# Kernel tuning notes

Measured on AMD Instinct MI355X. Metric: run time of the kernel, lower is better.

## Reference

```python
import jax, jax.numpy as jnp
import numpy as np

N_NODES = 50000
N_EDGES = 1600000
IN_FEATS = 128
HIDDEN = 32
HEADS = 4
N_GRAPHS = 64
NEG_SLOPE = 0.2


def setup_inputs() -> dict:
    key = jax.random.key(0)
    ks = jax.random.split(key, 10)
    features = jax.random.normal(ks[0], (N_NODES, IN_FEATS), dtype=jnp.float32)
    src = jax.random.randint(ks[1], (N_EDGES,), 0, N_NODES, dtype=jnp.int32)
    dst = jax.random.randint(ks[2], (N_EDGES,), 0, N_NODES, dtype=jnp.int32)
    graph_ids = jnp.sort(jax.random.randint(ks[3], (N_NODES,), 0, N_GRAPHS, dtype=jnp.int32))
    # GATConv params (fc has no bias in DGL; conv bias added post-aggregation)
    s = 1.0 / np.sqrt(IN_FEATS)
    W = jax.random.uniform(ks[4], (IN_FEATS, HEADS * HIDDEN), jnp.float32, -s, s)
    attn_l = jax.random.normal(ks[5], (HEADS, HIDDEN), dtype=jnp.float32) * 0.1
    attn_r = jax.random.normal(ks[6], (HEADS, HIDDEN), dtype=jnp.float32) * 0.1
    bias = jnp.zeros((HEADS * HIDDEN,), dtype=jnp.float32)
    s2 = 1.0 / np.sqrt(HEADS * HIDDEN)
    fc_w = jax.random.uniform(ks[7], (HEADS * HIDDEN, 1), jnp.float32, -s2, s2)
    fc_b = jnp.zeros((1,), dtype=jnp.float32)
    return dict(features=features, src=src, dst=dst, graph_ids=graph_ids,
                W=W, attn_l=attn_l, attn_r=attn_r, bias=bias, fc_w=fc_w, fc_b=fc_b)


def reference(features, src, dst, graph_ids, W, attn_l, attn_r, bias, fc_w, fc_b):
    N = features.shape[0]
    H, D = attn_l.shape
    feat = (features @ W).reshape(N, H, D)              # [N,H,D]
    el = jnp.sum(feat * attn_l[None], axis=-1)          # [N,H]
    er = jnp.sum(feat * attn_r[None], axis=-1)          # [N,H]
    e = jax.nn.leaky_relu(el[src] + er[dst], NEG_SLOPE) # [E,H]
    # edge softmax over incoming edges of each dst node
    m = jax.ops.segment_max(e, dst, num_segments=N)     # [N,H]
    ex = jnp.exp(e - m[dst])
    denom = jax.ops.segment_sum(ex, dst, num_segments=N)
    a = ex / denom[dst]                                 # [E,H]
    msg = feat[src] * a[:, :, None]                     # [E,H,D]
    rst = jax.ops.segment_sum(msg, dst, num_segments=N) # [N,H,D]
    h = rst.reshape(N, H * D) + bias[None, :]
    # dropout(p=0.5) treated as identity (eval mode)
    h = jax.nn.elu(h)
    counts = jax.ops.segment_sum(jnp.ones((N,), h.dtype), graph_ids, num_segments=N_GRAPHS)
    hg = jax.ops.segment_sum(h, graph_ids, num_segments=N_GRAPHS) / counts[:, None]
    y = jax.nn.sigmoid(hg @ fc_w + fc_b[None, :])       # [G,1]
    return y
```

## Files before the change

kernel.cpp:

```cpp
#include <hip/hip_runtime.h>
#include <hip/hip_bf16.h>
#include <math.h>

#define N_NODES 50000
#define N_EDGES 1600000
#define HEADS 4
#define HIDDEN 32
#define N_GRAPHS 64
#define NEG_SLOPE 0.2f

#define NBUCK 196
#define BKT_EPT 8
#define BKT_CHUNK (256 * BKT_EPT)
#define NBKB ((N_EDGES + BKT_CHUNK - 1) / BKT_CHUNK)

#define OFS_FEAT 0
#define OFS_EBUF 0
#define OFS_EL   6400000
#define OFS_ER   6600000
#define OFS_P    6800000
#define OFS_GCNT 6850000
#define OFS_GBASE 6850256
#define OFS_GPOS 6850512
#define OFS_WAB  6850768
#define OFS_OFF  6900000
#define OFS_SRC  6950272

typedef __attribute__((ext_vector_type(8))) short short8;
typedef __attribute__((ext_vector_type(4))) float f32x4;

#define LDS_S 68

__device__ __forceinline__ unsigned pack_bf16x2(float a, float b) {
  __hip_bfloat16 ha = __float2bfloat16(a), hb = __float2bfloat16(b);
  unsigned ua = *(const unsigned short*)&ha, ub = *(const unsigned short*)&hb;
  return ua | (ub << 16);
}
__device__ __forceinline__ float bf16_lo(unsigned u) {
  unsigned v = u << 16; return *(const float*)&v;
}
__device__ __forceinline__ float bf16_hi(unsigned u) {
  unsigned v = u & 0xFFFF0000u; return *(const float*)&v;
}

__global__ __launch_bounds__(1024) void k_wab(const float* __restrict__ W,
                                              const float* __restrict__ al,
                                              const float* __restrict__ ar,
                                              float* __restrict__ wab) {
  int t = threadIdx.x;
  int k = t >> 3, c = t & 7;
  int h = c & 3;
  const float* av = (c < 4) ? al : ar;
  float s = 0.f;
  for (int d = 0; d < 32; ++d)
    s = fmaf(W[k * 128 + h * 32 + d], av[h * 32 + d], s);
  wab[k * 8 + c] = s;
}

__global__ __launch_bounds__(256, 2) void k_gemm(
    const float* __restrict__ X, const float* __restrict__ W,
    const float* __restrict__ wab, unsigned* __restrict__ featb,
    float* __restrict__ el, float* __restrict__ er) {
  __shared__ unsigned Wt[144 * LDS_S];
  __shared__ unsigned Xt[64 * LDS_S];
  const int t = threadIdx.x;
  const int lane = t & 63;
  const int wv = t >> 6;
  const int nb0 = blockIdx.x * 64;

  {
    const int c = t & 127;
    const int ph = (t >> 7) * 32;
    for (int p = ph; p < ph + 32; ++p)
      Wt[c * LDS_S + p] = pack_bf16x2(W[(2 * p) * 128 + c], W[(2 * p + 1) * 128 + c]);
  }
  if (t < 128) {
    const int c = t & 7;
    const int p0 = (t >> 3) * 4;
    for (int q = 0; q < 4; ++q) {
      int p = p0 + q;
      Wt[(128 + c) * LDS_S + p] =
          pack_bf16x2(wab[(2 * p) * 8 + c], wab[(2 * p + 1) * 8 + c]);
    }
  } else {
    const int c = (t - 128) & 7;
    const int p0 = ((t - 128) >> 3) * 4;
    for (int q = 0; q < 4; ++q) Wt[(136 + c) * LDS_S + p0 + q] = 0;
  }
  {
    const int row = t >> 2;
    const int c0 = (t & 3) * 32;
    const int node = nb0 + row;
    const float4* xs = (const float4*)(X + (size_t)node * 128 + c0);
    for (int i = 0; i < 8; ++i) {
      float4 v = make_float4(0.f, 0.f, 0.f, 0.f);
      if (node < N_NODES) v = xs[i];
      int p = (c0 >> 1) + i * 2;
      Xt[row * LDS_S + p] = pack_bf16x2(v.x, v.y);
      Xt[row * LDS_S + p + 1] = pack_bf16x2(v.z, v.w);
    }
  }
  __syncthreads();

  const int rrow = lane & 15;
  const int rgrp = lane >> 4;
  f32x4 acc[9];
#pragma unroll
  for (int i = 0; i < 9; ++i) acc[i] = (f32x4){0.f, 0.f, 0.f, 0.f};
  const int arow = wv * 16 + rrow;

#pragma unroll
  for (int kk = 0; kk < 4; ++kk) {
    const int pbase = kk * 16 + rgrp * 4;
    short8 afrag = *(const short8*)&Xt[arow * LDS_S + pbase];
#pragma unroll
    for (int bt = 0; bt < 9; ++bt) {
      short8 bfrag = *(const short8*)&Wt[(bt * 16 + rrow) * LDS_S + pbase];
      acc[bt] = __builtin_amdgcn_mfma_f32_16x16x32_bf16(afrag, bfrag, acc[bt], 0, 0, 0);
    }
  }

  const int nodebase = nb0 + wv * 16 + rgrp * 4;
#pragma unroll
  for (int bt = 0; bt < 8; ++bt) {
#pragma unroll
    for (int j = 0; j < 4; ++j) {
      float other = __shfl_xor(acc[bt][j], 1, 64);
      if ((lane & 1) == 0) {
        int node = nodebase + j;
        if (node < N_NODES)
          featb[(size_t)node * 64 + bt * 8 + (rrow >> 1)] =
              pack_bf16x2(acc[bt][j], other);
      }
    }
  }
#pragma unroll
  for (int j = 0; j < 4; ++j) {
    int node = nodebase + j;
    if (node < N_NODES) {
      if (rrow < 4) el[node * 4 + rrow] = acc[8][j];
      else if (rrow < 8) er[node * 4 + (rrow - 4)] = acc[8][j];
    }
  }
}

__global__ void k_bhist(const int* __restrict__ dst, int* __restrict__ gcount) {
  __shared__ int lh[NBUCK];
  const int t = threadIdx.x;
  if (t < NBUCK) lh[t] = 0;
  __syncthreads();
  const int base = blockIdx.x * BKT_CHUNK;
#pragma unroll
  for (int j = 0; j < BKT_EPT; ++j) {
    int e = base + j * 256 + t;
    if (e < N_EDGES) atomicAdd(&lh[dst[e] >> 8], 1);
  }
  __syncthreads();
  if (t < NBUCK && lh[t] > 0) atomicAdd(&gcount[t], lh[t]);
}

__global__ void k_bscan(const int* __restrict__ gcount, int* __restrict__ gbase,
                        int* __restrict__ gpos) {
  __shared__ int sh[256];
  const int t = threadIdx.x;
  int v = (t < NBUCK) ? gcount[t] : 0;
  sh[t] = v;
  __syncthreads();
  for (int s = 1; s < 256; s <<= 1) {
    int add = (t >= s) ? sh[t - s] : 0;
    __syncthreads();
    sh[t] += add;
    __syncthreads();
  }
  int excl = sh[t] - v;
  if (t < NBUCK) { gbase[t] = excl; gpos[t] = excl; }
  if (t == NBUCK - 1) gbase[NBUCK] = excl + v;
}

__global__ void k_bucket(const int* __restrict__ src, const int* __restrict__ dst,
                         int* __restrict__ gpos, int2* __restrict__ ebuf) {
  __shared__ int lh[NBUCK];
  __shared__ int lbase[NBUCK];
  const int t = threadIdx.x;
  if (t < NBUCK) lh[t] = 0;
  __syncthreads();
  const int base = blockIdx.x * BKT_CHUNK;
  int s8[BKT_EPT], d8[BKT_EPT], r8[BKT_EPT], b8[BKT_EPT];
#pragma unroll
  for (int j = 0; j < BKT_EPT; ++j) {
    int e = base + j * 256 + t;
    bool ok = e < N_EDGES;
    s8[j] = ok ? src[e] : 0;
    d8[j] = ok ? dst[e] : 0;
    b8[j] = d8[j] >> 8;
    int r = 0;
    if (ok) r = atomicAdd(&lh[b8[j]], 1);
    r8[j] = r;
  }
  __syncthreads();
  if (t < NBUCK && lh[t] > 0) lbase[t] = atomicAdd(&gpos[t], lh[t]);
  __syncthreads();
#pragma unroll
  for (int j = 0; j < BKT_EPT; ++j) {
    int e = base + j * 256 + t;
    if (e < N_EDGES) ebuf[lbase[b8[j]] + r8[j]] = make_int2(s8[j], d8[j]);
  }
}

__global__ __launch_bounds__(1024) void k_bsort(
    const int2* __restrict__ ebuf, const int* __restrict__ gbase,
    int* __restrict__ srcbuf, int* __restrict__ off) {
  __shared__ int lcnt[256];
  __shared__ int loff[256];
  __shared__ int lpos[256];
  const int t = threadIdx.x;
  const int b = blockIdx.x;
  const int lo = gbase[b], hi = gbase[b + 1];
  if (t < 256) lcnt[t] = 0;
  __syncthreads();
  for (int i = lo + t; i < hi; i += 1024)
    atomicAdd(&lcnt[ebuf[i].y & 255], 1);
  __syncthreads();
  int v = (t < 256) ? lcnt[t] : 0;
  if (t < 256) loff[t] = v;
  __syncthreads();
  for (int s = 1; s < 256; s <<= 1) {
    int add = (t >= s && t < 256) ? loff[t - s] : 0;
    __syncthreads();
    if (t < 256) loff[t] += add;
    __syncthreads();
  }
  if (t < 256) {
    int excl = loff[t] - v;
    lpos[t] = excl;
    int node = b * 256 + t;
    if (node < N_NODES) off[node] = lo + excl;
  }
  if (b == NBUCK - 1 && t == 0) off[N_NODES] = N_EDGES;
  __syncthreads();
  for (int i = lo + t; i < hi; i += 1024) {
    int2 e = ebuf[i];
    int p = atomicAdd(&lpos[e.y & 255], 1);
    srcbuf[lo + p] = e.x;
  }
}

__global__ __launch_bounds__(256) void k_aggregate(
    const unsigned* __restrict__ featb, const float* __restrict__ el,
    const float* __restrict__ er, const int* __restrict__ off,
    const int* __restrict__ srcbuf, const float* __restrict__ bias,
    const float* __restrict__ fc_w, float* __restrict__ pbuf) {
  int gid = blockIdx.x * blockDim.x + threadIdx.x;
  int v = gid >> 6;
  if (v >= N_NODES) return;
  const int lane = threadIdx.x & 63;
  const int sub = lane & 15;
  const int par = lane >> 4;
  const int h = sub >> 2;

  const float erv = er[v * 4 + h];
  const int start = off[v], end = off[v + 1];

  float sum = 0.f;
  float acc0 = 0.f, acc1 = 0.f, acc2 = 0.f, acc3 = 0.f;
  float acc4 = 0.f, acc5 = 0.f, acc6 = 0.f, acc7 = 0.f;

  int iA = start + par;
  if (iA < end) {
    int sA = srcbuf[iA];
    float eA = el[sA * 4 + h];
    uint4 fA = *(const uint4*)&featb[(size_t)sA * 64 + sub * 4];

    int iB = iA + 4;
    bool hasB = iB < end;
    float eB = 0.f; uint4 fB = make_uint4(0, 0, 0, 0);
    if (hasB) {
      int sB = srcbuf[iB];
      eB = el[sB * 4 + h];
      fB = *(const uint4*)&featb[(size_t)sB * 64 + sub * 4];
    }

    while (true) {
      const int iC = iB + 4;
      const bool hasC = iC < end;
      float eC = 0.f; uint4 fC = make_uint4(0, 0, 0, 0);
      if (hasC) {
        int sC = srcbuf[iC];
        eC = el[sC * 4 + h];
        fC = *(const uint4*)&featb[(size_t)sC * 64 + sub * 4];
      }

      float e = eA + erv;
      e = (e > 0.f) ? e : NEG_SLOPE * e;
      float p = __expf(e);
      sum += p;
      acc0 = fmaf(bf16_lo(fA.x), p, acc0);
      acc1 = fmaf(bf16_hi(fA.x), p, acc1);
      acc2 = fmaf(bf16_lo(fA.y), p, acc2);
      acc3 = fmaf(bf16_hi(fA.y), p, acc3);
      acc4 = fmaf(bf16_lo(fA.z), p, acc4);
      acc5 = fmaf(bf16_hi(fA.z), p, acc5);
      acc6 = fmaf(bf16_lo(fA.w), p, acc6);
      acc7 = fmaf(bf16_hi(fA.w), p, acc7);

      if (!hasB) break;
      eA = eB; fA = fB;
      iB = iC; hasB = hasC; eB = eC; fB = fC;
    }
  }

#pragma unroll
  for (int mk = 16; mk < 64; mk <<= 1) {
    sum += __shfl_xor(sum, mk, 64);
    acc0 += __shfl_xor(acc0, mk, 64);
    acc1 += __shfl_xor(acc1, mk, 64);
    acc2 += __shfl_xor(acc2, mk, 64);
    acc3 += __shfl_xor(acc3, mk, 64);
    acc4 += __shfl_xor(acc4, mk, 64);
    acc5 += __shfl_xor(acc5, mk, 64);
    acc6 += __shfl_xor(acc6, mk, 64);
    acc7 += __shfl_xor(acc7, mk, 64);
  }

  const float inv = (end > start) ? 1.f / sum : 0.f;
  const float4 b4a = *(const float4*)&bias[sub * 8];
  const float4 b4b = *(const float4*)&bias[sub * 8 + 4];
  const float4 w4a = *(const float4*)&fc_w[sub * 8];
  const float4 w4b = *(const float4*)&fc_w[sub * 8 + 4];
  float r0 = fmaf(acc0, inv, b4a.x);
  float r1 = fmaf(acc1, inv, b4a.y);
  float r2 = fmaf(acc2, inv, b4a.z);
  float r3 = fmaf(acc3, inv, b4a.w);
  float r4 = fmaf(acc4, inv, b4b.x);
  float r5 = fmaf(acc5, inv, b4b.y);
  float r6 = fmaf(acc6, inv, b4b.z);
  float r7 = fmaf(acc7, inv, b4b.w);
  r0 = (r0 > 0.f) ? r0 : __expf(r0) - 1.f;
  r1 = (r1 > 0.f) ? r1 : __expf(r1) - 1.f;
  r2 = (r2 > 0.f) ? r2 : __expf(r2) - 1.f;
  r3 = (r3 > 0.f) ? r3 : __expf(r3) - 1.f;
  r4 = (r4 > 0.f) ? r4 : __expf(r4) - 1.f;
  r5 = (r5 > 0.f) ? r5 : __expf(r5) - 1.f;
  r6 = (r6 > 0.f) ? r6 : __expf(r6) - 1.f;
  r7 = (r7 > 0.f) ? r7 : __expf(r7) - 1.f;
  float t = r0 * w4a.x + r1 * w4a.y + r2 * w4a.z + r3 * w4a.w +
            r4 * w4b.x + r5 * w4b.y + r6 * w4b.z + r7 * w4b.w;
#pragma unroll
  for (int mk = 1; mk < 16; mk <<= 1) t += __shfl_xor(t, mk, 64);
  if (lane == 0) pbuf[v] = t;
}

__global__ void k_pool(const float* __restrict__ pbuf, const int* __restrict__ gids,
                       const float* __restrict__ fc_b, float* __restrict__ y) {
  int g = blockIdx.x;
  int a = 0, b = N_NODES;
  while (a < b) { int mid = (a + b) >> 1; if (gids[mid] < g) a = mid + 1; else b = mid; }
  int lo = a;
  b = N_NODES;
  while (a < b) { int mid = (a + b) >> 1; if (gids[mid] < g + 1) a = mid + 1; else b = mid; }
  int hi = a;

  float s = 0.f;
  for (int i = lo + threadIdx.x; i < hi; i += blockDim.x) s += pbuf[i];
  __shared__ float sh[256];
  sh[threadIdx.x] = s;
  __syncthreads();
  for (int st = 128; st > 0; st >>= 1) {
    if (threadIdx.x < st) sh[threadIdx.x] += sh[threadIdx.x + st];
    __syncthreads();
  }
  if (threadIdx.x == 0) {
    float cnt = (float)(hi - lo);
    float hg = sh[0] / cnt;
    float x = hg + fc_b[0];
    y[g] = 1.f / (1.f + expf(-x));
  }
}

extern "C" void kernel_launch(void* const* d_in, const int* in_sizes, int n_in,
                              void* d_out, int out_size, void* d_ws, size_t ws_size,
                              hipStream_t stream) {
  const float* features = (const float*)d_in[0];
  const int* src = (const int*)d_in[1];
  const int* dst = (const int*)d_in[2];
  const int* gids = (const int*)d_in[3];
  const float* W = (const float*)d_in[4];
  const float* attn_l = (const float*)d_in[5];
  const float* attn_r = (const float*)d_in[6];
  const float* bias = (const float*)d_in[7];
  const float* fc_w = (const float*)d_in[8];
  const float* fc_b = (const float*)d_in[9];

  float* ws = (float*)d_ws;
  unsigned* featb = (unsigned*)d_ws + OFS_FEAT;
  int2* ebuf = (int2*)((int*)d_ws + OFS_EBUF);
  float* el = ws + OFS_EL;
  float* er = ws + OFS_ER;
  float* pbuf = ws + OFS_P;
  int* gcount = (int*)d_ws + OFS_GCNT;
  int* gbase = (int*)d_ws + OFS_GBASE;
  int* gpos = (int*)d_ws + OFS_GPOS;
  float* wab = ws + OFS_WAB;
  int* off = (int*)d_ws + OFS_OFF;
  int* srcbuf = (int*)d_ws + OFS_SRC;

  hipMemsetAsync(gcount, 0, NBUCK * sizeof(int), stream);

  k_wab<<<1, 1024, 0, stream>>>(W, attn_l, attn_r, wab);

  k_bhist<<<NBKB, 256, 0, stream>>>(dst, gcount);
  k_bscan<<<1, 256, 0, stream>>>(gcount, gbase, gpos);
  k_bucket<<<NBKB, 256, 0, stream>>>(src, dst, gpos, ebuf);
  k_bsort<<<NBUCK, 1024, 0, stream>>>(ebuf, gbase, srcbuf, off);

  k_gemm<<<(N_NODES + 63) / 64, 256, 0, stream>>>(features, W, wab, featb, el, er);

  k_aggregate<<<(N_NODES * 64) / 256 + 1, 256, 0, stream>>>(featb, el, er, off, srcbuf,
                                                            bias, fc_w, pbuf);
  k_pool<<<N_GRAPHS, 256, 0, stream>>>(pbuf, gids, fc_b, (float*)d_out);
}
```

Baseline: 244.1 us.

## Store projected features as FP8 and pack edge buffer into 32-bit words

The projected node features are now stored as FP8 (e4m3) instead of bf16, which halves the bytes gathered per edge in the aggregation kernel. Hardware conversion builtins are used when available, with a software fallback. The bucket-sort edge buffer also packs a 16-bit source and the low 8 bits of dst into one 32-bit word instead of an int2. This cuts memory traffic in the gather-heavy aggregation and in the sort passes, but FP8 loses precision and the 16-bit source field cannot hold node ids of 65536 or more. N_NODES is 50000, so the packing holds only at this size.

```diff
diff --git a/kernel.cpp b/kernel.cpp
--- a/kernel.cpp
+++ b/kernel.cpp
@@ -28,19 +28,50 @@
 
 typedef __attribute__((ext_vector_type(8))) short short8;
 typedef __attribute__((ext_vector_type(4))) float f32x4;
+typedef __attribute__((ext_vector_type(2))) float f32x2;
 
 #define LDS_S 68
+
+#if __has_builtin(__builtin_amdgcn_cvt_pk_f32_fp8) && __has_builtin(__builtin_amdgcn_cvt_pk_fp8_f32)
+#define HAVE_HW_FP8 1
+#endif
 
 __device__ __forceinline__ unsigned pack_bf16x2(float a, float b) {
   __hip_bfloat16 ha = __float2bfloat16(a), hb = __float2bfloat16(b);
   unsigned ua = *(const unsigned short*)&ha, ub = *(const unsigned short*)&hb;
   return ua | (ub << 16);
 }
-__device__ __forceinline__ float bf16_lo(unsigned u) {
-  unsigned v = u << 16; return *(const float*)&v;
-}
-__device__ __forceinline__ float bf16_hi(unsigned u) {
-  unsigned v = u & 0xFFFF0000u; return *(const float*)&v;
+
+__device__ __forceinline__ void fp8x4_to_f32(unsigned u, float* o) {
+#ifdef HAVE_HW_FP8
+  f32x2 a = __builtin_amdgcn_cvt_pk_f32_fp8(u, false);
+  f32x2 b = __builtin_amdgcn_cvt_pk_f32_fp8(u, true);
+  o[0] = a[0]; o[1] = a[1]; o[2] = b[0]; o[3] = b[1];
+#else
+#pragma unroll
+  for (int k = 0; k < 4; ++k) {
+    unsigned byte = (u >> (8 * k)) & 0xFFu;
+    unsigned bits = ((byte & 0x80u) << 24) | ((byte & 0x7Fu) << 20);
+    o[k] = __uint_as_float(bits) * 0x1.0p+120f;
+  }
+#endif
+}
+#ifndef HAVE_HW_FP8
+__device__ __forceinline__ unsigned enc_fp8_1(float x) {
+  float y = x * 0x1.0p-120f;
+  unsigned u = __float_as_uint(y);
+  u += 0x7FFFFu + ((u >> 20) & 1u);
+  return ((u >> 24) & 0x80u) | ((u >> 20) & 0x7Fu);
+}
+#endif
+__device__ __forceinline__ unsigned f32x4_to_fp8(float a, float b, float c, float d) {
+#ifdef HAVE_HW_FP8
+  int u = __builtin_amdgcn_cvt_pk_fp8_f32(a, b, 0, false);
+  u = __builtin_amdgcn_cvt_pk_fp8_f32(c, d, u, true);
+  return (unsigned)u;
+#else
+  return enc_fp8_1(a) | (enc_fp8_1(b) << 8) | (enc_fp8_1(c) << 16) | (enc_fp8_1(d) << 24);
+#endif
 }
 
 __global__ __launch_bounds__(1024) void k_wab(const float* __restrict__ W,
@@ -125,12 +156,14 @@
   for (int bt = 0; bt < 8; ++bt) {
 #pragma unroll
     for (int j = 0; j < 4; ++j) {
-      float other = __shfl_xor(acc[bt][j], 1, 64);
-      if ((lane & 1) == 0) {
+      float v = acc[bt][j];
+      float x1 = __shfl_xor(v, 1, 64);
+      float x2 = __shfl_xor(v, 2, 64);
+      float x3 = __shfl_xor(v, 3, 64);
+      if ((rrow & 3) == 0) {
         int node = nodebase + j;
         if (node < N_NODES)
-          featb[(size_t)node * 64 + bt * 8 + (rrow >> 1)] =
-              pack_bf16x2(acc[bt][j], other);
+          featb[(size_t)node * 32 + bt * 4 + (rrow >> 2)] = f32x4_to_fp8(v, x1, x2, x3);
       }
     }
   }
@@ -178,7 +211,7 @@
 }
 
 __global__ void k_bucket(const int* __restrict__ src, const int* __restrict__ dst,
-                         int* __restrict__ gpos, int2* __restrict__ ebuf) {
+                         int* __restrict__ gpos, unsigned* __restrict__ ebuf) {
   __shared__ int lh[NBUCK];
   __shared__ int lbase[NBUCK];
   const int t = threadIdx.x;
@@ -203,12 +236,14 @@
 #pragma unroll
   for (int j = 0; j < BKT_EPT; ++j) {
     int e = base + j * 256 + t;
-    if (e < N_EDGES) ebuf[lbase[b8[j]] + r8[j]] = make_int2(s8[j], d8[j]);
+    if (e < N_EDGES)
+      ebuf[lbase[b8[j]] + r8[j]] =
+          (unsigned)s8[j] | ((unsigned)(d8[j] & 255) << 16);
   }
 }
 
 __global__ __launch_bounds__(1024) void k_bsort(
-    const int2* __restrict__ ebuf, const int* __restrict__ gbase,
+    const unsigned* __restrict__ ebuf, const int* __restrict__ gbase,
     int* __restrict__ srcbuf, int* __restrict__ off) {
   __shared__ int lcnt[256];
   __shared__ int loff[256];
@@ -219,7 +254,7 @@
   if (t < 256) lcnt[t] = 0;
   __syncthreads();
   for (int i = lo + t; i < hi; i += 1024)
-    atomicAdd(&lcnt[ebuf[i].y & 255], 1);
+    atomicAdd(&lcnt[(ebuf[i] >> 16) & 255], 1);
   __syncthreads();
   int v = (t < 256) ? lcnt[t] : 0;
   if (t < 256) loff[t] = v;
@@ -239,9 +274,9 @@
   if (b == NBUCK - 1 && t == 0) off[N_NODES] = N_EDGES;
   __syncthreads();
   for (int i = lo + t; i < hi; i += 1024) {
-    int2 e = ebuf[i];
-    int p = atomicAdd(&lpos[e.y & 255], 1);
-    srcbuf[lo + p] = e.x;
+    unsigned e = ebuf[i];
+    int p = atomicAdd(&lpos[(e >> 16) & 255], 1);
+    srcbuf[lo + p] = (int)(e & 0xFFFFu);
   }
 }
 
@@ -269,39 +304,42 @@
   if (iA < end) {
     int sA = srcbuf[iA];
     float eA = el[sA * 4 + h];
-    uint4 fA = *(const uint4*)&featb[(size_t)sA * 64 + sub * 4];
+    uint2 fA = *(const uint2*)&featb[(size_t)sA * 32 + sub * 2];
 
     int iB = iA + 4;
     bool hasB = iB < end;
-    float eB = 0.f; uint4 fB = make_uint4(0, 0, 0, 0);
+    float eB = 0.f; uint2 fB = make_uint2(0, 0);
     if (hasB) {
       int sB = srcbuf[iB];
       eB = el[sB * 4 + h];
-      fB = *(const uint4*)&featb[(size_t)sB * 64 + sub * 4];
+      fB = *(const uint2*)&featb[(size_t)sB * 32 + sub * 2];
     }
 
     while (true) {
       const int iC = iB + 4;
       const bool hasC = iC < end;
-      float eC = 0.f; uint4 fC = make_uint4(0, 0, 0, 0);
+      float eC = 0.f; uint2 fC = make_uint2(0, 0);
       if (hasC) {
         int sC = srcbuf[iC];
         eC = el[sC * 4 + h];
-        fC = *(const uint4*)&featb[(size_t)sC * 64 + sub * 4];
+        fC = *(const uint2*)&featb[(size_t)sC * 32 + sub * 2];
       }
 
       float e = eA + erv;
       e = (e > 0.f) ? e : NEG_SLOPE * e;
       float p = __expf(e);
       sum += p;
-      acc0 = fmaf(bf16_lo(fA.x), p, acc0);
-      acc1 = fmaf(bf16_hi(fA.x), p, acc1);
-      acc2 = fmaf(bf16_lo(fA.y), p, acc2);
-      acc3 = fmaf(bf16_hi(fA.y), p, acc3);
-      acc4 = fmaf(bf16_lo(fA.z), p, acc4);
-      acc5 = fmaf(bf16_hi(fA.z), p, acc5);
-      acc6 = fmaf(bf16_lo(fA.w), p, acc6);
-      acc7 = fmaf(bf16_hi(fA.w), p, acc7);
+      float fv[8];
+      fp8x4_to_f32(fA.x, fv);
+      fp8x4_to_f32(fA.y, fv + 4);
+      acc0 = fmaf(fv[0], p, acc0);
+      acc1 = fmaf(fv[1], p, acc1);
+      acc2 = fmaf(fv[2], p, acc2);
+      acc3 = fmaf(fv[3], p, acc3);
+      acc4 = fmaf(fv[4], p, acc4);
+      acc5 = fmaf(fv[5], p, acc5);
+      acc6 = fmaf(fv[6], p, acc6);
+      acc7 = fmaf(fv[7], p, acc7);
 
       if (!hasB) break;
       eA = eB; fA = fB;
@@ -393,7 +431,7 @@
 
   float* ws = (float*)d_ws;
   unsigned* featb = (unsigned*)d_ws + OFS_FEAT;
-  int2* ebuf = (int2*)((int*)d_ws + OFS_EBUF);
+  unsigned* ebuf = (unsigned*)d_ws + OFS_EBUF;
   float* el = ws + OFS_EL;
   float* er = ws + OFS_ER;
   float* pbuf = ws + OFS_P;
```

Measured after the change: 236.9 us. 1.03x faster.
